# Kernel tuning notes

Measured on AMD Instinct MI355X. Metric: run time of the kernel, lower is better.

The kernel has to match this reference:

```python
import jax, jax.numpy as jnp
import numpy as np

N = 100000   # nodes
E = 1600000  # edges
IN = 768     # in_dim
H = 128      # hidden_dim
G = 64       # graphs per batch


def setup_inputs() -> dict:
    key = jax.random.key(0)
    ks = jax.random.split(key, 9)
    x = jax.random.normal(ks[0], (N, IN), jnp.float32)
    edge_index = jax.random.randint(ks[1], (2, E), 0, N, dtype=jnp.int64)
    batch = jnp.sort(jax.random.randint(ks[2], (N,), 0, G, dtype=jnp.int64))
    W1 = jax.random.normal(ks[3], (IN, H), jnp.float32) / np.float32(np.sqrt(IN))
    b1 = jax.random.normal(ks[4], (H,), jnp.float32) * 0.01
    W2 = jax.random.normal(ks[5], (H, H), jnp.float32) / np.float32(np.sqrt(H))
    b2 = jax.random.normal(ks[6], (H,), jnp.float32) * 0.01
    Wh = jax.random.normal(ks[7], (H, 2), jnp.float32) / np.float32(np.sqrt(H))
    bh = jax.random.normal(ks[8], (2,), jnp.float32) * 0.01
    return dict(x=x, edge_index=edge_index, batch=batch, W1=W1, b1=b1,
                W2=W2, b2=b2, Wh=Wh, bh=bh, num_graphs=G)


def gcn_conv(x, src, dst, W, b, n):
    # PyG GCNConv default: add self-loops (already in src/dst), symmetric norm.
    deg = jax.ops.segment_sum(jnp.ones_like(dst, x.dtype), dst, num_segments=n)
    dis = jnp.where(deg > 0, jax.lax.rsqrt(deg), jnp.zeros_like(deg))
    h = x @ W                                   # [n, out]
    norm = (dis[src] * dis[dst])[:, None]       # [E+n, 1]
    out = jax.ops.segment_sum(h[src] * norm, dst, num_segments=n)
    return out + b


def reference(x, edge_index, batch, W1, b1, W2, b2, Wh, bh, num_graphs):
    n = x.shape[0]
    loop = jnp.arange(n, dtype=edge_index.dtype)
    src = jnp.concatenate([edge_index[0], loop])
    dst = jnp.concatenate([edge_index[1], loop])
    h = jax.nn.relu(gcn_conv(x, src, dst, W1, b1, n))   # dropout = eval identity
    h = jax.nn.relu(gcn_conv(h, src, dst, W2, b2, n))
    summed = jax.ops.segment_sum(h, batch, num_segments=num_graphs)
    counts = jax.ops.segment_sum(jnp.ones((n, 1), h.dtype), batch, num_segments=num_graphs)
    emb = summed / jnp.maximum(counts, 1.0)             # global_mean_pool
    return emb @ Wh + bh
```

## Files before the change

kernel.cpp:

```cpp
#include <hip/hip_runtime.h>
#include <hip/hip_bf16.h>

static constexpr int N_NODES  = 100000;
static constexpr int N_EDGES  = 1600000;
static constexpr int DIM_IN   = 768;
static constexpr int DIM_H    = 128;
static constexpr int N_GRAPHS = 64;
static constexpr int NB_SCAN  = (N_NODES + 255) / 256;

typedef __attribute__((ext_vector_type(8))) short short8;
typedef __attribute__((ext_vector_type(4))) float f32x4;

__device__ __forceinline__ ushort f2bf(float f) {
    union { float f; uint u; } v; v.f = f;
    uint r = v.u + 0x7fffu + ((v.u >> 16) & 1u);
    return (ushort)(r >> 16);
}
__device__ __forceinline__ float bf2f(ushort u) {
    union { uint u; float f; } v; v.u = ((uint)u) << 16;
    return v.f;
}

__global__ void k_indeg(const int* __restrict__ edst, int* __restrict__ indeg) {
    int e = blockIdx.x * 256 + threadIdx.x;
    if (e < N_EDGES) atomicAdd(&indeg[edst[e]], 1);
}

__global__ void k_scan1(const int* __restrict__ indeg, int* __restrict__ rp,
                        int* __restrict__ bsum, float* __restrict__ dis) {
    __shared__ int s[256];
    int t = threadIdx.x;
    int i = blockIdx.x * 256 + t;
    int v = (i < N_NODES) ? indeg[i] : 0;
    s[t] = v;
    __syncthreads();
    for (int off = 1; off < 256; off <<= 1) {
        int x = (t >= off) ? s[t - off] : 0;
        __syncthreads();
        s[t] += x;
        __syncthreads();
    }
    if (i < N_NODES) {
        rp[i] = s[t] - v;
        dis[i] = rsqrtf((float)v + 1.0f);
    }
    if (t == 255) bsum[blockIdx.x] = s[255];
}

__global__ void k_scan2(int* __restrict__ bsum, const int* __restrict__ batch,
                        int* __restrict__ gstart) {
    __shared__ int s[512];
    int t = threadIdx.x;
    int v = (t < NB_SCAN) ? bsum[t] : 0;
    s[t] = v;
    __syncthreads();
    for (int off = 1; off < 512; off <<= 1) {
        int x = (t >= off) ? s[t - off] : 0;
        __syncthreads();
        s[t] += x;
        __syncthreads();
    }
    if (t < NB_SCAN) bsum[t] = s[t] - v;
    if (t <= N_GRAPHS) {
        int lo = 0, hi = N_NODES;
        while (lo < hi) {
            int mid = (lo + hi) >> 1;
            if (batch[mid] < t) lo = mid + 1; else hi = mid;
        }
        gstart[t] = lo;
    }
}

__global__ void k_scatter(const int* __restrict__ esrc, const int* __restrict__ edst,
                          const int* __restrict__ rp, const int* __restrict__ bsum,
                          const float* __restrict__ dis,
                          int* __restrict__ cursor, uint2* __restrict__ csrw) {
    int e = blockIdx.x * 256 + threadIdx.x;
    if (e >= N_EDGES) return;
    int d = edst[e];
    int sv = esrc[e];
    int pos = atomicAdd(&cursor[d], 1);
    uint2 val;
    val.x = (uint)sv;
    val.y = __float_as_uint(dis[sv]);
    csrw[rp[d] + bsum[d >> 8] + pos] = val;
}

__global__ void k_convW(const float* __restrict__ W1, const float* __restrict__ W2,
                        ushort* __restrict__ W1th, ushort* __restrict__ W1tl,
                        ushort* __restrict__ W2th, ushort* __restrict__ W2tl) {
    int i = blockIdx.x * 256 + threadIdx.x;
    const int total1 = DIM_IN * DIM_H;
    if (i < total1) {
        int k = i >> 7, n = i & 127;
        float w = W1[i];
        ushort h = f2bf(w);
        ushort lo = f2bf(w - bf2f(h));
        W1th[(size_t)n * DIM_IN + k] = h;
        W1tl[(size_t)n * DIM_IN + k] = lo;
    } else {
        int j = i - total1;
        if (j < DIM_H * DIM_H) {
            int k = j >> 7, n = j & 127;
            float w = W2[j];
            ushort h = f2bf(w);
            ushort lo = f2bf(w - bf2f(h));
            W2th[(size_t)n * DIM_H + k] = h;
            W2tl[(size_t)n * DIM_H + k] = lo;
        }
    }
}

#define LDSTR 40

template<int K, bool AFP32>
__global__ __launch_bounds__(256) void k_gemm_mfma(const void* __restrict__ Av,
                                                   const ushort* __restrict__ Wth,
                                                   const ushort* __restrict__ Wtl,
                                                   ushort* __restrict__ C,
                                                   int nrows) {
    __shared__ ushort As[128 * LDSTR];
    __shared__ ushort Bh[128 * LDSTR];
    __shared__ ushort Bl[128 * LDSTR];

    const int t = threadIdx.x;
    const int row0 = blockIdx.x * 128;
    const int srow = t >> 1;
    const int skoff = (t & 1) * 16;
    const int l = t & 63;
    const int wv = t >> 6;
    const int wm = wv >> 1, wn = wv & 1;
    const int lr = l & 15;
    const int lk = (l >> 4) * 8;

    f32x4 acc[4][4];
    const f32x4 zero = {0.f, 0.f, 0.f, 0.f};
    #pragma unroll
    for (int m = 0; m < 4; ++m)
        #pragma unroll
        for (int n = 0; n < 4; ++n) acc[m][n] = zero;

    for (int k0 = 0; k0 < K; k0 += 32) {
        {
            uint p[8];
            if (AFP32) {
                float f[16];
                if (row0 + srow < nrows) {
                    const float4* Ap = (const float4*)((const float*)Av +
                        (size_t)(row0 + srow) * K + k0 + skoff);
                    *(float4*)&f[0]  = Ap[0];
                    *(float4*)&f[4]  = Ap[1];
                    *(float4*)&f[8]  = Ap[2];
                    *(float4*)&f[12] = Ap[3];
                } else {
                    #pragma unroll
                    for (int i = 0; i < 16; ++i) f[i] = 0.f;
                }
                #pragma unroll
                for (int i = 0; i < 8; ++i)
                    p[i] = (uint)f2bf(f[2 * i]) | ((uint)f2bf(f[2 * i + 1]) << 16);
            } else {
                uint4 q0 = {0, 0, 0, 0}, q1 = {0, 0, 0, 0};
                if (row0 + srow < nrows) {
                    const uint4* Ap = (const uint4*)((const ushort*)Av +
                        (size_t)(row0 + srow) * K + k0 + skoff);
                    q0 = Ap[0]; q1 = Ap[1];
                }
                p[0] = q0.x; p[1] = q0.y; p[2] = q0.z; p[3] = q0.w;
                p[4] = q1.x; p[5] = q1.y; p[6] = q1.z; p[7] = q1.w;
            }
            uint4 w0 = {p[0], p[1], p[2], p[3]};
            uint4 w1 = {p[4], p[5], p[6], p[7]};
            *(uint4*)&As[srow * LDSTR + skoff]     = w0;
            *(uint4*)&As[srow * LDSTR + skoff + 8] = w1;
        }
        {
            const uint4* Wp = (const uint4*)(Wth + (size_t)srow * K + k0 + skoff);
            *(uint4*)&Bh[srow * LDSTR + skoff]     = Wp[0];
            *(uint4*)&Bh[srow * LDSTR + skoff + 8] = Wp[1];
            const uint4* Wq = (const uint4*)(Wtl + (size_t)srow * K + k0 + skoff);
            *(uint4*)&Bl[srow * LDSTR + skoff]     = Wq[0];
            *(uint4*)&Bl[srow * LDSTR + skoff + 8] = Wq[1];
        }
        __syncthreads();

        short8 a[4], bh[4], bl[4];
        #pragma unroll
        for (int m = 0; m < 4; ++m)
            a[m] = *(const short8*)&As[(wm * 64 + m * 16 + lr) * LDSTR + lk];
        #pragma unroll
        for (int n = 0; n < 4; ++n) {
            bh[n] = *(const short8*)&Bh[(wn * 64 + n * 16 + lr) * LDSTR + lk];
            bl[n] = *(const short8*)&Bl[(wn * 64 + n * 16 + lr) * LDSTR + lk];
        }
        #pragma unroll
        for (int m = 0; m < 4; ++m)
            #pragma unroll
            for (int n = 0; n < 4; ++n) {
                acc[m][n] = __builtin_amdgcn_mfma_f32_16x16x32_bf16(a[m], bh[n], acc[m][n], 0, 0, 0);
                acc[m][n] = __builtin_amdgcn_mfma_f32_16x16x32_bf16(a[m], bl[n], acc[m][n], 0, 0, 0);
            }
        __syncthreads();
    }

    #pragma unroll
    for (int m = 0; m < 4; ++m) {
        #pragma unroll
        for (int n = 0; n < 4; ++n) {
            int col = wn * 64 + n * 16 + lr;
            #pragma unroll
            for (int j = 0; j < 4; ++j) {
                int row = row0 + wm * 64 + m * 16 + (l >> 4) * 4 + j;
                if (row < nrows)
                    C[(size_t)row * DIM_H + col] = f2bf(acc[m][n][j]);
            }
        }
    }
}

__device__ __forceinline__ void acc8(uint4 u, float w, float* a) {
    a[0] += bf2f((ushort)(u.x & 0xffff)) * w;
    a[1] += bf2f((ushort)(u.x >> 16))    * w;
    a[2] += bf2f((ushort)(u.y & 0xffff)) * w;
    a[3] += bf2f((ushort)(u.y >> 16))    * w;
    a[4] += bf2f((ushort)(u.z & 0xffff)) * w;
    a[5] += bf2f((ushort)(u.z >> 16))    * w;
    a[6] += bf2f((ushort)(u.w & 0xffff)) * w;
    a[7] += bf2f((ushort)(u.w >> 16))    * w;
}

__global__ __launch_bounds__(256) void k_agg(const ushort* __restrict__ hin,
                                             const uint2* __restrict__ csrw,
                                             const int* __restrict__ rp,
                                             const int* __restrict__ bsum,
                                             const int* __restrict__ indeg,
                                             const float* __restrict__ dis,
                                             const float* __restrict__ bias,
                                             ushort* __restrict__ hout) {
    int node = (blockIdx.x * 256 + threadIdx.x) >> 6;
    int lane = threadIdx.x & 63;
    if (node >= N_NODES) return;
    int q  = lane >> 4;
    int cl = lane & 15;
    float di = dis[node];
    int beg = rp[node] + bsum[node >> 8];
    int cnt = indeg[node];

    float a[8] = {0.f, 0.f, 0.f, 0.f, 0.f, 0.f, 0.f, 0.f};

    {
        uint s; float w;
        if (q == 0)             { s = (uint)node; w = di * di; }
        else if (q - 1 < cnt)   { uint2 p = csrw[beg + q - 1]; s = p.x; w = __uint_as_float(p.y) * di; }
        else                    { s = (uint)node; w = 0.f; }
        uint4 u = ((const uint4*)(hin + (size_t)s * DIM_H))[cl];
        acc8(u, w, a);
    }
    const uint2* cp = csrw + beg + 3;
    int m = cnt - 3;
    int i = 0;
    for (; i + 8 <= m; i += 8) {
        uint2 p0 = cp[i + q];
        uint2 p1 = cp[i + 4 + q];
        float w0 = __uint_as_float(p0.y) * di;
        float w1 = __uint_as_float(p1.y) * di;
        uint4 u0 = ((const uint4*)(hin + (size_t)p0.x * DIM_H))[cl];
        uint4 u1 = ((const uint4*)(hin + (size_t)p1.x * DIM_H))[cl];
        acc8(u0, w0, a);
        acc8(u1, w1, a);
    }
    for (; i < m; i += 4) {
        int idx = i + q;
        uint s; float w;
        if (idx < m) { uint2 p = cp[idx]; s = p.x; w = __uint_as_float(p.y) * di; }
        else         { s = (uint)node;    w = 0.f; }
        uint4 u = ((const uint4*)(hin + (size_t)s * DIM_H))[cl];
        acc8(u, w, a);
    }

    #pragma unroll
    for (int j = 0; j < 8; ++j) {
        a[j] += __shfl_xor(a[j], 16);
        a[j] += __shfl_xor(a[j], 32);
    }

    if (q == 0) {
        float4 b0 = ((const float4*)bias)[cl * 2];
        float4 b1 = ((const float4*)bias)[cl * 2 + 1];
        float o0 = fmaxf(a[0] + b0.x, 0.f), o1 = fmaxf(a[1] + b0.y, 0.f);
        float o2 = fmaxf(a[2] + b0.z, 0.f), o3 = fmaxf(a[3] + b0.w, 0.f);
        float o4 = fmaxf(a[4] + b1.x, 0.f), o5 = fmaxf(a[5] + b1.y, 0.f);
        float o6 = fmaxf(a[6] + b1.z, 0.f), o7 = fmaxf(a[7] + b1.w, 0.f);
        uint4 o;
        o.x = (uint)f2bf(o0) | ((uint)f2bf(o1) << 16);
        o.y = (uint)f2bf(o2) | ((uint)f2bf(o3) << 16);
        o.z = (uint)f2bf(o4) | ((uint)f2bf(o5) << 16);
        o.w = (uint)f2bf(o6) | ((uint)f2bf(o7) << 16);
        ((uint4*)(hout + (size_t)node * DIM_H))[cl] = o;
    }
}

#define PSPLIT 8
__global__ __launch_bounds__(256) void k_pool(const ushort* __restrict__ h,
                                              const int* __restrict__ gstart,
                                              float* __restrict__ pooled2) {
    int g  = blockIdx.x >> 3;
    int sp = blockIdx.x & 7;
    int r0 = gstart[g], r1 = gstart[g + 1];
    int count = r1 - r0;
    int chunk = (count + PSPLIT - 1) / PSPLIT;
    int aS = r0 + sp * chunk;
    int bE = min(aS + chunk, r1);
    int c  = threadIdx.x & 63;
    int rr = threadIdx.x >> 6;
    float s0 = 0.f, s1 = 0.f;
    for (int r = aS + rr; r < bE; r += 4) {
        uint u = ((const uint*)(h + (size_t)r * DIM_H))[c];
        s0 += bf2f((ushort)(u & 0xffff));
        s1 += bf2f((ushort)(u >> 16));
    }
    __shared__ float sm0[4][64], sm1[4][64];
    sm0[rr][c] = s0; sm1[rr][c] = s1;
    __syncthreads();
    if (rr == 0) {
        float v0 = sm0[0][c] + sm0[1][c] + sm0[2][c] + sm0[3][c];
        float v1 = sm1[0][c] + sm1[1][c] + sm1[2][c] + sm1[3][c];
        float* dst = pooled2 + (size_t)(g * PSPLIT + sp) * DIM_H;
        dst[2 * c]     = v0;
        dst[2 * c + 1] = v1;
    }
}

__global__ __launch_bounds__(128) void k_head(const float* __restrict__ pooled2,
                                              const int* __restrict__ gstart,
                                              const float* __restrict__ Wh,
                                              const float* __restrict__ bh,
                                              float* __restrict__ out) {
    int g = blockIdx.x;
    int c = threadIdx.x;
    float s = 0.f;
    #pragma unroll
    for (int sp = 0; sp < PSPLIT; ++sp)
        s += pooled2[(size_t)(g * PSPLIT + sp) * DIM_H + c];
    float cntg = (float)(gstart[g + 1] - gstart[g]);
    float e = s / fmaxf(cntg, 1.0f);
    __shared__ float s0[128], s1[128];
    s0[c] = e * Wh[c * 2 + 0];
    s1[c] = e * Wh[c * 2 + 1];
    __syncthreads();
    for (int off = 64; off > 0; off >>= 1) {
        if (c < off) { s0[c] += s0[c + off]; s1[c] += s1[c + off]; }
        __syncthreads();
    }
    if (c == 0) {
        out[g * 2 + 0] = s0[0] + bh[0];
        out[g * 2 + 1] = s1[0] + bh[1];
    }
}

extern "C" void kernel_launch(void* const* d_in, const int* in_sizes, int n_in,
                              void* d_out, int out_size, void* d_ws, size_t ws_size,
                              hipStream_t stream) {
    const float* x    = (const float*)d_in[0];
    const int*   esrc = (const int*)d_in[1];
    const int*   edst = esrc + N_EDGES;
    const int*   batch= (const int*)d_in[2];
    const float* W1   = (const float*)d_in[3];
    const float* b1   = (const float*)d_in[4];
    const float* W2   = (const float*)d_in[5];
    const float* b2   = (const float*)d_in[6];
    const float* Wh   = (const float*)d_in[7];
    const float* bh   = (const float*)d_in[8];
    float* out = (float*)d_out;

    char* ws = (char*)d_ws;
    size_t off = 0;
    auto alloc = [&](size_t bytes) {
        void* p = ws + off;
        off += (bytes + 255) & ~(size_t)255;
        return p;
    };
    ushort* bufZ   = (ushort*)alloc((size_t)N_NODES * DIM_H * 2);
    ushort* bufH   = (ushort*)alloc((size_t)N_NODES * DIM_H * 2);
    float*  dis    = (float*)alloc((size_t)N_NODES * 4);
    int*    deg2   = (int*)  alloc((size_t)2 * N_NODES * 4);
    int*    indeg  = deg2;
    int*    cursor = deg2 + N_NODES;
    int*    rp     = (int*)  alloc((size_t)N_NODES * 4);
    uint2*  csrw   = (uint2*)alloc((size_t)N_EDGES * 8);
    int*    bsum   = (int*)  alloc(512 * 4);
    float*  pooled2= (float*)alloc((size_t)N_GRAPHS * PSPLIT * DIM_H * 4);
    int*    gstart = (int*)  alloc((N_GRAPHS + 1) * 4);
    ushort* W1th   = (ushort*)alloc((size_t)DIM_IN * DIM_H * 2);
    ushort* W1tl   = (ushort*)alloc((size_t)DIM_IN * DIM_H * 2);
    ushort* W2th   = (ushort*)alloc((size_t)DIM_H * DIM_H * 2);
    ushort* W2tl   = (ushort*)alloc((size_t)DIM_H * DIM_H * 2);

    hipMemsetAsync(deg2, 0, (size_t)2 * N_NODES * 4, stream);

    int convblocks = (DIM_IN * DIM_H + DIM_H * DIM_H + 255) / 256;
    k_convW  <<<convblocks, 256, 0, stream>>>(W1, W2, W1th, W1tl, W2th, W2tl);

    k_indeg  <<<(N_EDGES + 255) / 256, 256, 0, stream>>>(edst, indeg);
    k_scan1  <<<NB_SCAN, 256, 0, stream>>>(indeg, rp, bsum, dis);
    k_scan2  <<<1, 512, 0, stream>>>(bsum, batch, gstart);
    k_scatter<<<(N_EDGES + 255) / 256, 256, 0, stream>>>(esrc, edst, rp, bsum, dis, cursor, csrw);

    int gblocks = (N_NODES + 127) / 128;
    k_gemm_mfma<DIM_IN, true ><<<gblocks, 256, 0, stream>>>(x,    W1th, W1tl, bufZ, N_NODES);
    k_agg<<<(N_NODES + 3) / 4, 256, 0, stream>>>(bufZ, csrw, rp, bsum, indeg, dis, b1, bufH);
    k_gemm_mfma<DIM_H,  false><<<gblocks, 256, 0, stream>>>(bufH, W2th, W2tl, bufZ, N_NODES);
    k_agg<<<(N_NODES + 3) / 4, 256, 0, stream>>>(bufZ, csrw, rp, bsum, indeg, dis, b2, bufH);

    k_pool<<<N_GRAPHS * PSPLIT, 256, 0, stream>>>(bufH, gstart, pooled2);
    k_head<<<N_GRAPHS, 128, 0, stream>>>(pooled2, gstart, Wh, bh, out);
}
```

Before: 453.4 us.

## Fuse preprocessing and pool/head kernels, prefetch GEMM A tiles, pipeline aggregation loads

Merges the weight conversion and in-degree counting into one launch, and pool plus head into a single per-graph kernel, removing two launches and the pooled intermediate buffer. The GEMM now prefetches the next A tile into registers and uses the hardware packed bf16 convert instruction. The aggregation loop is restructured into a uniform software-pipelined loop with the self-loop folded in, so neighbour indices are loaded one step ahead. The pool kernel now runs only 64 blocks, which lowers parallelism for the pooling pass.

Result: slower. 539.5 us (+19.0%).

```diff
diff --git a/kernel.cpp b/kernel.cpp
--- a/kernel.cpp
+++ b/kernel.cpp
@@ -20,10 +20,35 @@
     union { uint u; float f; } v; v.u = ((uint)u) << 16;
     return v.f;
 }
-
-__global__ void k_indeg(const int* __restrict__ edst, int* __restrict__ indeg) {
-    int e = blockIdx.x * 256 + threadIdx.x;
-    if (e < N_EDGES) atomicAdd(&indeg[edst[e]], 1);
+__device__ __forceinline__ uint cvtpk(float lo, float hi) {
+    uint r;
+    asm("v_cvt_pk_bf16_f32 %0, %1, %2" : "=v"(r) : "v"(lo), "v"(hi));
+    return r;
+}
+
+__global__ void k_pre(const float* __restrict__ W1, const float* __restrict__ W2,
+                      ushort* __restrict__ W1th, ushort* __restrict__ W1tl,
+                      ushort* __restrict__ W2th, ushort* __restrict__ W2tl,
+                      const int* __restrict__ edst, int* __restrict__ indeg) {
+    int i = blockIdx.x * 256 + threadIdx.x;
+    if (i < N_EDGES) atomicAdd(&indeg[edst[i]], 1);
+    const int total1 = DIM_IN * DIM_H;
+    if (i < total1) {
+        int k = i >> 7, n = i & 127;
+        float w = W1[i];
+        ushort h = f2bf(w);
+        ushort lo = f2bf(w - bf2f(h));
+        W1th[(size_t)n * DIM_IN + k] = h;
+        W1tl[(size_t)n * DIM_IN + k] = lo;
+    } else if (i < total1 + DIM_H * DIM_H) {
+        int j = i - total1;
+        int k = j >> 7, n = j & 127;
+        float w = W2[j];
+        ushort h = f2bf(w);
+        ushort lo = f2bf(w - bf2f(h));
+        W2th[(size_t)n * DIM_H + k] = h;
+        W2tl[(size_t)n * DIM_H + k] = lo;
+    }
 }
 
 __global__ void k_scan1(const int* __restrict__ indeg, int* __restrict__ rp,
@@ -86,31 +111,6 @@
     csrw[rp[d] + bsum[d >> 8] + pos] = val;
 }
 
-__global__ void k_convW(const float* __restrict__ W1, const float* __restrict__ W2,
-                        ushort* __restrict__ W1th, ushort* __restrict__ W1tl,
-                        ushort* __restrict__ W2th, ushort* __restrict__ W2tl) {
-    int i = blockIdx.x * 256 + threadIdx.x;
-    const int total1 = DIM_IN * DIM_H;
-    if (i < total1) {
-        int k = i >> 7, n = i & 127;
-        float w = W1[i];
-        ushort h = f2bf(w);
-        ushort lo = f2bf(w - bf2f(h));
-        W1th[(size_t)n * DIM_IN + k] = h;
-        W1tl[(size_t)n * DIM_IN + k] = lo;
-    } else {
-        int j = i - total1;
-        if (j < DIM_H * DIM_H) {
-            int k = j >> 7, n = j & 127;
-            float w = W2[j];
-            ushort h = f2bf(w);
-            ushort lo = f2bf(w - bf2f(h));
-            W2th[(size_t)n * DIM_H + k] = h;
-            W2tl[(size_t)n * DIM_H + k] = lo;
-        }
-    }
-}
-
 #define LDSTR 40
 
 template<int K, bool AFP32>
@@ -132,6 +132,7 @@
     const int wm = wv >> 1, wn = wv & 1;
     const int lr = l & 15;
     const int lk = (l >> 4) * 8;
+    const bool arow_ok = (row0 + srow < nrows);
 
     f32x4 acc[4][4];
     const f32x4 zero = {0.f, 0.f, 0.f, 0.f};
@@ -140,48 +141,56 @@
         #pragma unroll
         for (int n = 0; n < 4; ++n) acc[m][n] = zero;
 
+    float4 fa[4];
+    uint4  ha[2];
+
+    auto loadA = [&](int k0) {
+        if (AFP32) {
+            if (arow_ok) {
+                const float4* p = (const float4*)((const float*)Av +
+                    (size_t)(row0 + srow) * K + k0 + skoff);
+                fa[0] = p[0]; fa[1] = p[1]; fa[2] = p[2]; fa[3] = p[3];
+            } else {
+                float4 z = {0.f, 0.f, 0.f, 0.f};
+                fa[0] = z; fa[1] = z; fa[2] = z; fa[3] = z;
+            }
+        } else {
+            if (arow_ok) {
+                const uint4* p = (const uint4*)((const ushort*)Av +
+                    (size_t)(row0 + srow) * K + k0 + skoff);
+                ha[0] = p[0]; ha[1] = p[1];
+            } else {
+                uint4 z = {0, 0, 0, 0};
+                ha[0] = z; ha[1] = z;
+            }
+        }
+    };
+
+    loadA(0);
     for (int k0 = 0; k0 < K; k0 += 32) {
-        {
-            uint p[8];
-            if (AFP32) {
-                float f[16];
-                if (row0 + srow < nrows) {
-                    const float4* Ap = (const float4*)((const float*)Av +
-                        (size_t)(row0 + srow) * K + k0 + skoff);
-                    *(float4*)&f[0]  = Ap[0];
-                    *(float4*)&f[4]  = Ap[1];
-                    *(float4*)&f[8]  = Ap[2];
-                    *(float4*)&f[12] = Ap[3];
-                } else {
-                    #pragma unroll
-                    for (int i = 0; i < 16; ++i) f[i] = 0.f;
-                }
-                #pragma unroll
-                for (int i = 0; i < 8; ++i)
-                    p[i] = (uint)f2bf(f[2 * i]) | ((uint)f2bf(f[2 * i + 1]) << 16);
-            } else {
-                uint4 q0 = {0, 0, 0, 0}, q1 = {0, 0, 0, 0};
-                if (row0 + srow < nrows) {
-                    const uint4* Ap = (const uint4*)((const ushort*)Av +
-                        (size_t)(row0 + srow) * K + k0 + skoff);
-                    q0 = Ap[0]; q1 = Ap[1];
-                }
-                p[0] = q0.x; p[1] = q0.y; p[2] = q0.z; p[3] = q0.w;
-                p[4] = q1.x; p[5] = q1.y; p[6] = q1.z; p[7] = q1.w;
-            }
-            uint4 w0 = {p[0], p[1], p[2], p[3]};
-            uint4 w1 = {p[4], p[5], p[6], p[7]};
+        const uint4* Wp = (const uint4*)(Wth + (size_t)srow * K + k0 + skoff);
+        uint4 wh0 = Wp[0], wh1 = Wp[1];
+        const uint4* Wq = (const uint4*)(Wtl + (size_t)srow * K + k0 + skoff);
+        uint4 wl0 = Wq[0], wl1 = Wq[1];
+
+        if (AFP32) {
+            uint4 w0, w1;
+            w0.x = cvtpk(fa[0].x, fa[0].y); w0.y = cvtpk(fa[0].z, fa[0].w);
+            w0.z = cvtpk(fa[1].x, fa[1].y); w0.w = cvtpk(fa[1].z, fa[1].w);
+            w1.x = cvtpk(fa[2].x, fa[2].y); w1.y = cvtpk(fa[2].z, fa[2].w);
+            w1.z = cvtpk(fa[3].x, fa[3].y); w1.w = cvtpk(fa[3].z, fa[3].w);
             *(uint4*)&As[srow * LDSTR + skoff]     = w0;
             *(uint4*)&As[srow * LDSTR + skoff + 8] = w1;
-        }
-        {
-            const uint4* Wp = (const uint4*)(Wth + (size_t)srow * K + k0 + skoff);
-            *(uint4*)&Bh[srow * LDSTR + skoff]     = Wp[0];
-            *(uint4*)&Bh[srow * LDSTR + skoff + 8] = Wp[1];
-            const uint4* Wq = (const uint4*)(Wtl + (size_t)srow * K + k0 + skoff);
-            *(uint4*)&Bl[srow * LDSTR + skoff]     = Wq[0];
-            *(uint4*)&Bl[srow * LDSTR + skoff + 8] = Wq[1];
-        }
+        } else {
+            *(uint4*)&As[srow * LDSTR + skoff]     = ha[0];
+            *(uint4*)&As[srow * LDSTR + skoff + 8] = ha[1];
+        }
+        if (k0 + 32 < K) loadA(k0 + 32);
+
+        *(uint4*)&Bh[srow * LDSTR + skoff]     = wh0;
+        *(uint4*)&Bh[srow * LDSTR + skoff + 8] = wh1;
+        *(uint4*)&Bl[srow * LDSTR + skoff]     = wl0;
+        *(uint4*)&Bl[srow * LDSTR + skoff + 8] = wl1;
         __syncthreads();
 
         short8 a[4], bh[4], bl[4];
@@ -245,37 +254,28 @@
     float di = dis[node];
     int beg = rp[node] + bsum[node >> 8];
     int cnt = indeg[node];
+    int T = cnt + 1;
+    const uint2* cp = csrw + beg - 1;
+
+    auto lp = [&](int idx) -> uint2 {
+        uint2 r;
+        if (idx > 0 && idx < T) { r = cp[idx]; }
+        else if (idx == 0)      { r.x = (uint)node; r.y = __float_as_uint(di); }
+        else                    { r.x = (uint)node; r.y = 0u; }
+        return r;
+    };
 
     float a[8] = {0.f, 0.f, 0.f, 0.f, 0.f, 0.f, 0.f, 0.f};
 
-    {
-        uint s; float w;
-        if (q == 0)             { s = (uint)node; w = di * di; }
-        else if (q - 1 < cnt)   { uint2 p = csrw[beg + q - 1]; s = p.x; w = __uint_as_float(p.y) * di; }
-        else                    { s = (uint)node; w = 0.f; }
-        uint4 u = ((const uint4*)(hin + (size_t)s * DIM_H))[cl];
-        acc8(u, w, a);
-    }
-    const uint2* cp = csrw + beg + 3;
-    int m = cnt - 3;
-    int i = 0;
-    for (; i + 8 <= m; i += 8) {
-        uint2 p0 = cp[i + q];
-        uint2 p1 = cp[i + 4 + q];
-        float w0 = __uint_as_float(p0.y) * di;
-        float w1 = __uint_as_float(p1.y) * di;
-        uint4 u0 = ((const uint4*)(hin + (size_t)p0.x * DIM_H))[cl];
-        uint4 u1 = ((const uint4*)(hin + (size_t)p1.x * DIM_H))[cl];
-        acc8(u0, w0, a);
-        acc8(u1, w1, a);
-    }
-    for (; i < m; i += 4) {
-        int idx = i + q;
-        uint s; float w;
-        if (idx < m) { uint2 p = cp[idx]; s = p.x; w = __uint_as_float(p.y) * di; }
-        else         { s = (uint)node;    w = 0.f; }
-        uint4 u = ((const uint4*)(hin + (size_t)s * DIM_H))[cl];
-        acc8(u, w, a);
+    uint2 A0 = lp(q), A1 = lp(4 + q);
+    for (int b = 0; b < T; b += 8) {
+        uint2 B0 = lp(b + 8 + q);
+        uint2 B1 = lp(b + 12 + q);
+        uint4 u0 = ((const uint4*)(hin + (size_t)A0.x * DIM_H))[cl];
+        uint4 u1 = ((const uint4*)(hin + (size_t)A1.x * DIM_H))[cl];
+        acc8(u0, __uint_as_float(A0.y) * di, a);
+        acc8(u1, __uint_as_float(A1.y) * di, a);
+        A0 = B0; A1 = B1;
     }
 
     #pragma unroll
@@ -300,21 +300,17 @@
     }
 }
 
-#define PSPLIT 8
-__global__ __launch_bounds__(256) void k_pool(const ushort* __restrict__ h,
-                                              const int* __restrict__ gstart,
-                                              float* __restrict__ pooled2) {
-    int g  = blockIdx.x >> 3;
-    int sp = blockIdx.x & 7;
+__global__ __launch_bounds__(256) void k_poolhead(const ushort* __restrict__ h,
+                                                  const int* __restrict__ gstart,
+                                                  const float* __restrict__ Wh,
+                                                  const float* __restrict__ bh,
+                                                  float* __restrict__ out) {
+    int g = blockIdx.x;
     int r0 = gstart[g], r1 = gstart[g + 1];
-    int count = r1 - r0;
-    int chunk = (count + PSPLIT - 1) / PSPLIT;
-    int aS = r0 + sp * chunk;
-    int bE = min(aS + chunk, r1);
     int c  = threadIdx.x & 63;
     int rr = threadIdx.x >> 6;
     float s0 = 0.f, s1 = 0.f;
-    for (int r = aS + rr; r < bE; r += 4) {
+    for (int r = r0 + rr; r < r1; r += 4) {
         uint u = ((const uint*)(h + (size_t)r * DIM_H))[c];
         s0 += bf2f((ushort)(u & 0xffff));
         s1 += bf2f((ushort)(u >> 16));
@@ -322,39 +318,22 @@
     __shared__ float sm0[4][64], sm1[4][64];
     sm0[rr][c] = s0; sm1[rr][c] = s1;
     __syncthreads();
-    if (rr == 0) {
+    if (threadIdx.x < 64) {
         float v0 = sm0[0][c] + sm0[1][c] + sm0[2][c] + sm0[3][c];
         float v1 = sm1[0][c] + sm1[1][c] + sm1[2][c] + sm1[3][c];
-        float* dst = pooled2 + (size_t)(g * PSPLIT + sp) * DIM_H;
-        dst[2 * c]     = v0;
-        dst[2 * c + 1] = v1;
-    }
-}
-
-__global__ __launch_bounds__(128) void k_head(const float* __restrict__ pooled2,
-                                              const int* __restrict__ gstart,
-                                              const float* __restrict__ Wh,
-                                              const float* __restrict__ bh,
-                                              float* __restrict__ out) {
-    int g = blockIdx.x;
-    int c = threadIdx.x;
-    float s = 0.f;
-    #pragma unroll
-    for (int sp = 0; sp < PSPLIT; ++sp)
-        s += pooled2[(size_t)(g * PSPLIT + sp) * DIM_H + c];
-    float cntg = (float)(gstart[g + 1] - gstart[g]);
-    float e = s / fmaxf(cntg, 1.0f);
-    __shared__ float s0[128], s1[128];
-    s0[c] = e * Wh[c * 2 + 0];
-    s1[c] = e * Wh[c * 2 + 1];
-    __syncthreads();
-    for (int off = 64; off > 0; off >>= 1) {
-        if (c < off) { s0[c] += s0[c + off]; s1[c] += s1[c + off]; }
-        __syncthreads();
-    }
-    if (c == 0) {
-        out[g * 2 + 0] = s0[0] + bh[0];
-        out[g * 2 + 1] = s1[0] + bh[1];
+        float inv = 1.f / fmaxf((float)(r1 - r0), 1.f);
+        float e0 = v0 * inv, e1 = v1 * inv;
+        float g0 = e0 * Wh[(2 * c) * 2 + 0] + e1 * Wh[(2 * c + 1) * 2 + 0];
+        float g1 = e0 * Wh[(2 * c) * 2 + 1] + e1 * Wh[(2 * c + 1) * 2 + 1];
+        #pragma unroll
+        for (int off = 32; off > 0; off >>= 1) {
+            g0 += __shfl_down(g0, off);
+            g1 += __shfl_down(g1, off);
+        }
+        if (c == 0) {
+            out[g * 2 + 0] = g0 + bh[0];
+            out[g * 2 + 1] = g1 + bh[1];
+        }
     }
 }
 
@@ -389,7 +368,6 @@
     int*    rp     = (int*)  alloc((size_t)N_NODES * 4);
     uint2*  csrw   = (uint2*)alloc((size_t)N_EDGES * 8);
     int*    bsum   = (int*)  alloc(512 * 4);
-    float*  pooled2= (float*)alloc((size_t)N_GRAPHS * PSPLIT * DIM_H * 4);
     int*    gstart = (int*)  alloc((N_GRAPHS + 1) * 4);
     ushort* W1th   = (ushort*)alloc((size_t)DIM_IN * DIM_H * 2);
     ushort* W1tl   = (ushort*)alloc((size_t)DIM_IN * DIM_H * 2);
@@ -398,10 +376,8 @@
 
     hipMemsetAsync(deg2, 0, (size_t)2 * N_NODES * 4, stream);
 
-    int convblocks = (DIM_IN * DIM_H + DIM_H * DIM_H + 255) / 256;
-    k_convW  <<<convblocks, 256, 0, stream>>>(W1, W2, W1th, W1tl, W2th, W2tl);
-
-    k_indeg  <<<(N_EDGES + 255) / 256, 256, 0, stream>>>(edst, indeg);
+    k_pre    <<<(N_EDGES + 255) / 256, 256, 0, stream>>>(W1, W2, W1th, W1tl, W2th, W2tl,
+                                                         edst, indeg);
     k_scan1  <<<NB_SCAN, 256, 0, stream>>>(indeg, rp, bsum, dis);
     k_scan2  <<<1, 512, 0, stream>>>(bsum, batch, gstart);
     k_scatter<<<(N_EDGES + 255) / 256, 256, 0, stream>>>(esrc, edst, rp, bsum, dis, cursor, csrw);
@@ -412,6 +388,5 @@
     k_gemm_mfma<DIM_H,  false><<<gblocks, 256, 0, stream>>>(bufH, W2th, W2tl, bufZ, N_NODES);
     k_agg<<<(N_NODES + 3) / 4, 256, 0, stream>>>(bufZ, csrw, rp, bsum, indeg, dis, b2, bufH);
 
-    k_pool<<<N_GRAPHS * PSPLIT, 256, 0, stream>>>(bufH, gstart, pooled2);
-    k_head<<<N_GRAPHS, 128, 0, stream>>>(pooled2, gstart, Wh, bh, out);
-}
+    k_poolhead<<<N_GRAPHS, 256, 0, stream>>>(bufH, gstart, Wh, bh, out);
+}
```
